# Kernel tuning notes

Hardware: AMD Instinct MI355X
Metric: run time of the kernel (lower is better)

The kernel has to match this reference:

```python
import jax, jax.numpy as jnp
import numpy as np

E = 8        # num experts
K = 2        # top-k
B, L, D = 2, 2048, 2048
I = 768      # moe expert intermediate size
IS = 4096    # shared expert intermediate size


def setup_inputs() -> dict:
    key = jax.random.key(0)
    ks = jax.random.split(key, 8)
    s = 0.02
    return {
        "hidden_states": jax.random.normal(ks[0], (B, L, D), jnp.float32),
        "gate_w": jax.random.normal(ks[1], (E, D), jnp.float32) * s,
        "gate_up_proj": jax.random.normal(ks[2], (E, 2 * I, D), jnp.float32) * s,
        "down_proj": jax.random.normal(ks[3], (E, D, I), jnp.float32) * s,
        "shared_gate_w": jax.random.normal(ks[4], (IS, D), jnp.float32) * s,
        "shared_up_w": jax.random.normal(ks[5], (IS, D), jnp.float32) * s,
        "shared_down_w": jax.random.normal(ks[6], (D, IS), jnp.float32) * s,
        "shared_expert_gate_w": jax.random.normal(ks[7], (1, D), jnp.float32) * s,
    }


def reference(hidden_states, gate_w, gate_up_proj, down_proj,
              shared_gate_w, shared_up_w, shared_down_w, shared_expert_gate_w):
    Bb, Ll, Dd = hidden_states.shape
    h = hidden_states.reshape(-1, Dd)                         # [T, D]
    silu = jax.nn.silu

    # shared expert: SiLU-gated MLP, scaled by sigmoid scalar gate
    shared = (silu(h @ shared_gate_w.T) * (h @ shared_up_w.T)) @ shared_down_w.T
    shared_out = jax.nn.sigmoid(h @ shared_expert_gate_w.T) * shared   # [T, D]

    # router: softmax over all experts, top-k, renormalize
    logits = h @ gate_w.T                                     # [T, E]
    probs = jax.nn.softmax(logits, axis=-1)
    topk_w, topk_idx = jax.lax.top_k(probs, K)                # [T, K]
    topk_w = topk_w / jnp.sum(topk_w, axis=-1, keepdims=True)

    # combine weights per (token, expert); zero for unselected experts,
    # so the dense per-expert compute below matches the gather/scatter loop.
    cw = jnp.sum(jax.nn.one_hot(topk_idx, E, dtype=h.dtype) * topk_w[..., None], axis=1)  # [T, E]

    # grouped gated MLP over all experts (dense dispatch)
    gu = jnp.einsum('td,efd->tef', h, gate_up_proj)           # [T, E, 2I]
    g, u = jnp.split(gu, 2, axis=-1)
    act = silu(g) * u                                         # [T, E, I]
    out = jnp.einsum('tei,edi->ted', act, down_proj)          # [T, E, D]
    partial = jnp.einsum('ted,te->td', out, cw)               # [T, D]

    return (partial + shared_out).reshape(Bb, Ll, Dd)
```

## Files before the change

### kernel.cpp

```cpp
#include <hip/hip_runtime.h>


#define T_TOK 4096
#define DIM   2048
#define NEXP  8
#define IEXP  768
#define ISHR  4096

typedef __attribute__((ext_vector_type(8))) short bf16x8_t;
typedef __attribute__((ext_vector_type(4))) float f32x4_t;

__device__ __forceinline__ unsigned short f2bf(float f) {
    unsigned int u = __float_as_uint(f);
    u += 0x7fffu + ((u >> 16) & 1u);
    return (unsigned short)(u >> 16);
}

__device__ __forceinline__ void gl2lds16(const unsigned short* g, unsigned short* l) {
    __builtin_amdgcn_global_load_lds(
        (const __attribute__((address_space(1))) unsigned int*)g,
        (__attribute__((address_space(3))) unsigned int*)l, 16, 0, 0);
}

#define C0 6291456
#define C1 9437184
#define C2 11534336
#define C3 13631488
#define C4 15728640
__global__ __launch_bounds__(256) void fused_cast_kernel(
    const float* __restrict__ s0, const float* __restrict__ s1,
    const float* __restrict__ s2, const float* __restrict__ s3,
    const float* __restrict__ s4,
    unsigned short* __restrict__ d0, unsigned short* __restrict__ d1,
    unsigned short* __restrict__ d2, unsigned short* __restrict__ d3,
    unsigned short* __restrict__ d4, int* __restrict__ cnt) {
    if (blockIdx.x == 0 && threadIdx.x < NEXP) cnt[threadIdx.x] = 0;
    int i = blockIdx.x * 256 + threadIdx.x;
    const float* src; unsigned short* dst; int base;
    if      (i < C0) { src = s0; dst = d0; base = 0;  }
    else if (i < C1) { src = s1; dst = d1; base = C0; }
    else if (i < C2) { src = s2; dst = d2; base = C1; }
    else if (i < C3) { src = s3; dst = d3; base = C2; }
    else             { src = s4; dst = d4; base = C3; }
    int j = i - base;
    float4 v = ((const float4*)src)[j];
    short4 r;
    r.x = (short)f2bf(v.x); r.y = (short)f2bf(v.y);
    r.z = (short)f2bf(v.z); r.w = (short)f2bf(v.w);
    ((short4*)dst)[j] = r;
}

__global__ __launch_bounds__(256) void router_kernel(
    const float* __restrict__ h, const float* __restrict__ gw,
    const float* __restrict__ segw,
    unsigned short* __restrict__ h_bf,
    float* __restrict__ sig, int* __restrict__ cnt,
    int* __restrict__ enc, float* __restrict__ wl) {
    int w = threadIdx.x >> 6, l = threadIdx.x & 63;
    int t = blockIdx.x * 4 + w;
    float p[9];
#pragma unroll
    for (int e = 0; e < 9; ++e) p[e] = 0.f;
    const float* hr = h + (size_t)t * DIM;
    unsigned short* hb = h_bf + (size_t)t * DIM;
    for (int i = 0; i < DIM; i += 64) {
        float x = hr[i + l];
        hb[i + l] = f2bf(x);
#pragma unroll
        for (int e = 0; e < NEXP; ++e) p[e] += x * gw[e * DIM + i + l];
        p[8] += x * segw[i + l];
    }
#pragma unroll
    for (int off = 32; off > 0; off >>= 1) {
#pragma unroll
        for (int e = 0; e < 9; ++e) p[e] += __shfl_xor(p[e], off, 64);
    }
    if (l == 0) {
        int b1 = 0; float v1 = p[0];
        for (int e = 1; e < NEXP; ++e) if (p[e] > v1) { v1 = p[e]; b1 = e; }
        int b2 = -1; float v2 = -1e30f;
        for (int e = 0; e < NEXP; ++e)
            if (e != b1 && p[e] > v2) { v2 = p[e]; b2 = e; }
        float w1 = 1.f / (1.f + __expf(v2 - v1));
        int pos = atomicAdd(&cnt[b1], 1);
        enc[b1 * T_TOK + pos] = 2 * t;     wl[b1 * T_TOK + pos] = w1;
        pos = atomicAdd(&cnt[b2], 1);
        enc[b2 * T_TOK + pos] = 2 * t + 1; wl[b2 * T_TOK + pos] = 1.f - w1;
        sig[t] = 1.f / (1.f + __expf(-p[8]));
    }
}


__global__ __launch_bounds__(64, 2) void gemm_gateup_all(
    const unsigned short* __restrict__ hA,
    const unsigned short* __restrict__ wsg, const unsigned short* __restrict__ wsu,
    const unsigned short* __restrict__ wgu,
    const int* __restrict__ enc, const int* __restrict__ cnt_arr,
    unsigned short* __restrict__ act_s, unsigned short* __restrict__ act_e) {
    int z = blockIdx.z;
    const unsigned short *Wg, *Wu;
    const int* lst; int cnt, gc0, ldo;
    unsigned short* outp;
    if (z < 128) {
        gc0 = z * 32; Wg = wsg; Wu = wsu;
        lst = nullptr; cnt = T_TOK; outp = act_s; ldo = ISHR;
    } else {
        int zz = z - 128;
        int e = zz / 24, ny = zz % 24;
        gc0 = ny * 32;
        Wg = wgu + (size_t)e * 2 * IEXP * DIM;
        Wu = Wg + (size_t)IEXP * DIM;
        lst = enc + e * T_TOK; cnt = cnt_arr[e];
        outp = act_e + (size_t)e * T_TOK * IEXP; ldo = IEXP;
    }
    int m0 = blockIdx.x * 64;
    if (m0 >= cnt) return;

    __shared__ __align__(16) unsigned short As[64 * 64];
    __shared__ __align__(16) unsigned short Bs[64 * 64];

    int l = threadIdx.x;
    int subrow = l >> 3;
    int chunk8 = ((l & 7) ^ subrow) << 3;

    unsigned aoff[8];
    unsigned boff[8];
#pragma unroll
    for (int c = 0; c < 8; ++c) {
        int row = 8 * c + subrow;
        int pp = m0 + row; if (pp >= cnt) pp = cnt - 1;
        int tk = lst ? (lst[pp] >> 1) : pp;
        aoff[c] = (unsigned)(tk * DIM + chunk8);
        int rg = row >> 4;
        int wrow = gc0 + ((rg >> 1) << 4) + (row & 15);
        boff[c] = (unsigned)(wrow * DIM + chunk8);
    }

    f32x4_t zero4 = {0.f, 0.f, 0.f, 0.f};
    f32x4_t acc[4][4];
#pragma unroll
    for (int i = 0; i < 4; ++i)
#pragma unroll
        for (int j = 0; j < 4; ++j) acc[i][j] = zero4;

    int lane15 = l & 15, q = l >> 4;

#pragma unroll
    for (int c = 0; c < 8; ++c) {
        gl2lds16(hA + aoff[c], &As[c * 512]);
        gl2lds16((((c >> 1) & 1) ? Wu : Wg) + boff[c], &Bs[c * 512]);
    }

    const int NK = DIM / 64;
    for (int t = 0; t < NK; ++t) {
        asm volatile("s_waitcnt vmcnt(0)" ::: "memory");
        __builtin_amdgcn_sched_barrier(0);
        bf16x8_t a[4][2], b[4][2];
#pragma unroll
        for (int i = 0; i < 4; ++i) {
            int R = 16 * i + lane15;
            int base = R * 64;
            int sx = (R & 7) << 3;
#pragma unroll
            for (int kk = 0; kk < 2; ++kk) {
                int cx = (((kk * 4 + q) << 3) ^ sx);
                a[i][kk] = *(const bf16x8_t*)&As[base + cx];
                b[i][kk] = *(const bf16x8_t*)&Bs[base + cx];
            }
        }
        asm volatile("s_waitcnt lgkmcnt(0)" ::: "memory");
        __builtin_amdgcn_sched_barrier(0);
        if (t + 1 < NK) {
            int k1 = (t + 1) * 64;
#pragma unroll
            for (int c = 0; c < 8; ++c) {
                gl2lds16(hA + aoff[c] + k1, &As[c * 512]);
                gl2lds16((((c >> 1) & 1) ? Wu : Wg) + boff[c] + k1, &Bs[c * 512]);
            }
        }
        __builtin_amdgcn_sched_barrier(0);
#pragma unroll
        for (int kk = 0; kk < 2; ++kk)
#pragma unroll
            for (int i = 0; i < 4; ++i)
#pragma unroll
                for (int j = 0; j < 4; ++j)
                    acc[i][j] = __builtin_amdgcn_mfma_f32_16x16x32_bf16(
                        a[i][kk], b[j][kk], acc[i][j], 0, 0, 0);
    }

#pragma unroll
    for (int i = 0; i < 4; ++i) {
#pragma unroll
        for (int r = 0; r < 4; ++r) {
            int p = m0 + 16 * i + 4 * q + r;
            unsigned short* orow = outp + (size_t)p * ldo + gc0 + lane15;
            float g0 = acc[i][0][r], u0 = acc[i][1][r];
            float g1 = acc[i][2][r], u1 = acc[i][3][r];
            orow[0]  = f2bf((g0 / (1.f + __expf(-g0))) * u0);
            orow[16] = f2bf((g1 / (1.f + __expf(-g1))) * u1);
        }
    }
}

__global__ __launch_bounds__(64, 2) void gemm_down_shared(
    const unsigned short* __restrict__ act_s,
    const unsigned short* __restrict__ wsd,
    const float* __restrict__ sig,
    float* __restrict__ out) {
    int m0 = blockIdx.x * 64;
    int n0 = blockIdx.y * 64;

    __shared__ __align__(16) unsigned short As[64 * 64];
    __shared__ __align__(16) unsigned short Bs[64 * 64];

    int l = threadIdx.x;
    int subrow = l >> 3;
    int chunk8 = ((l & 7) ^ subrow) << 3;

    unsigned aoff[8], boff[8];
#pragma unroll
    for (int c = 0; c < 8; ++c) {
        int row = 8 * c + subrow;
        aoff[c] = (unsigned)((m0 + row) * ISHR + chunk8);
        boff[c] = (unsigned)((n0 + row) * ISHR + chunk8);
    }

    f32x4_t zero4 = {0.f, 0.f, 0.f, 0.f};
    f32x4_t acc[4][4];
#pragma unroll
    for (int i = 0; i < 4; ++i)
#pragma unroll
        for (int j = 0; j < 4; ++j) acc[i][j] = zero4;

    int lane15 = l & 15, q = l >> 4;

#pragma unroll
    for (int c = 0; c < 8; ++c) {
        gl2lds16(act_s + aoff[c], &As[c * 512]);
        gl2lds16(wsd + boff[c], &Bs[c * 512]);
    }

    const int NK = ISHR / 64;
    for (int t = 0; t < NK; ++t) {
        asm volatile("s_waitcnt vmcnt(0)" ::: "memory");
        __builtin_amdgcn_sched_barrier(0);
        bf16x8_t a[4][2], b[4][2];
#pragma unroll
        for (int i = 0; i < 4; ++i) {
            int R = 16 * i + lane15;
            int base = R * 64;
            int sx = (R & 7) << 3;
#pragma unroll
            for (int kk = 0; kk < 2; ++kk) {
                int cx = (((kk * 4 + q) << 3) ^ sx);
                a[i][kk] = *(const bf16x8_t*)&As[base + cx];
                b[i][kk] = *(const bf16x8_t*)&Bs[base + cx];
            }
        }
        asm volatile("s_waitcnt lgkmcnt(0)" ::: "memory");
        __builtin_amdgcn_sched_barrier(0);
        if (t + 1 < NK) {
            int k1 = (t + 1) * 64;
#pragma unroll
            for (int c = 0; c < 8; ++c) {
                gl2lds16(act_s + aoff[c] + k1, &As[c * 512]);
                gl2lds16(wsd + boff[c] + k1, &Bs[c * 512]);
            }
        }
        __builtin_amdgcn_sched_barrier(0);
#pragma unroll
        for (int kk = 0; kk < 2; ++kk)
#pragma unroll
            for (int i = 0; i < 4; ++i)
#pragma unroll
                for (int j = 0; j < 4; ++j)
                    acc[i][j] = __builtin_amdgcn_mfma_f32_16x16x32_bf16(
                        a[i][kk], b[j][kk], acc[i][j], 0, 0, 0);
    }

#pragma unroll
    for (int i = 0; i < 4; ++i) {
#pragma unroll
        for (int r = 0; r < 4; ++r) {
            int p = m0 + 16 * i + 4 * q + r;
            float sc = sig[p];
            float* orow = out + (size_t)p * DIM + n0 + lane15;
#pragma unroll
            for (int j = 0; j < 4; ++j)
                orow[16 * j] = sc * acc[i][j][r];
        }
    }
}

__global__ __launch_bounds__(64, 2) void gemm_down_expert(
    const unsigned short* __restrict__ act_e,
    const unsigned short* __restrict__ wdn,
    const int* __restrict__ enc, const int* __restrict__ cnt_arr,
    const float* __restrict__ wlst,
    float* __restrict__ out) {
    int e = blockIdx.z;
    const unsigned short* A = act_e + (size_t)e * T_TOK * IEXP;
    const unsigned short* W = wdn + (size_t)e * DIM * IEXP;
    const int* lst = enc + e * T_TOK;
    const float* scl = wlst + (size_t)e * T_TOK;
    int cnt = cnt_arr[e];
    int m0 = blockIdx.x * 64;
    if (m0 >= cnt) return;
    int n0 = blockIdx.y * 64;

    __shared__ __align__(16) unsigned short As[64 * 64];
    __shared__ __align__(16) unsigned short Bs[64 * 64];

    int l = threadIdx.x;
    int subrow = l >> 3;
    int chunk8 = ((l & 7) ^ subrow) << 3;

    unsigned aoff[8], boff[8];
#pragma unroll
    for (int c = 0; c < 8; ++c) {
        int row = 8 * c + subrow;
        int pp = m0 + row; if (pp >= cnt) pp = cnt - 1;
        aoff[c] = (unsigned)(pp * IEXP + chunk8);
        boff[c] = (unsigned)((n0 + row) * IEXP + chunk8);
    }

    f32x4_t zero4 = {0.f, 0.f, 0.f, 0.f};
    f32x4_t acc[4][4];
#pragma unroll
    for (int i = 0; i < 4; ++i)
#pragma unroll
        for (int j = 0; j < 4; ++j) acc[i][j] = zero4;

    int lane15 = l & 15, q = l >> 4;

#pragma unroll
    for (int c = 0; c < 8; ++c) {
        gl2lds16(A + aoff[c], &As[c * 512]);
        gl2lds16(W + boff[c], &Bs[c * 512]);
    }

    const int NK = IEXP / 64;
    for (int t = 0; t < NK; ++t) {
        asm volatile("s_waitcnt vmcnt(0)" ::: "memory");
        __builtin_amdgcn_sched_barrier(0);
        bf16x8_t a[4][2], b[4][2];
#pragma unroll
        for (int i = 0; i < 4; ++i) {
            int R = 16 * i + lane15;
            int base = R * 64;
            int sx = (R & 7) << 3;
#pragma unroll
            for (int kk = 0; kk < 2; ++kk) {
                int cx = (((kk * 4 + q) << 3) ^ sx);
                a[i][kk] = *(const bf16x8_t*)&As[base + cx];
                b[i][kk] = *(const bf16x8_t*)&Bs[base + cx];
            }
        }
        asm volatile("s_waitcnt lgkmcnt(0)" ::: "memory");
        __builtin_amdgcn_sched_barrier(0);
        if (t + 1 < NK) {
            int k1 = (t + 1) * 64;
#pragma unroll
            for (int c = 0; c < 8; ++c) {
                gl2lds16(A + aoff[c] + k1, &As[c * 512]);
                gl2lds16(W + boff[c] + k1, &Bs[c * 512]);
            }
        }
        __builtin_amdgcn_sched_barrier(0);
#pragma unroll
        for (int kk = 0; kk < 2; ++kk)
#pragma unroll
            for (int i = 0; i < 4; ++i)
#pragma unroll
                for (int j = 0; j < 4; ++j)
                    acc[i][j] = __builtin_amdgcn_mfma_f32_16x16x32_bf16(
                        a[i][kk], b[j][kk], acc[i][j], 0, 0, 0);
    }

#pragma unroll
    for (int i = 0; i < 4; ++i) {
#pragma unroll
        for (int r = 0; r < 4; ++r) {
            int p = m0 + 16 * i + 4 * q + r;
            if (p < cnt) {
                int dest = lst[p] >> 1;
                float sc = scl[p];
                float* orow = out + (size_t)dest * DIM + n0 + lane15;
#pragma unroll
                for (int j = 0; j < 4; ++j)
                    atomicAdd(&orow[16 * j], sc * acc[i][j][r]);
            }
        }
    }
}

extern "C" void kernel_launch(void* const* d_in, const int* in_sizes, int n_in,
                              void* d_out, int out_size, void* d_ws, size_t ws_size,
                              hipStream_t stream) {
    (void)in_sizes; (void)n_in; (void)out_size; (void)ws_size;
    const float* h    = (const float*)d_in[0];
    const float* gw   = (const float*)d_in[1];
    const float* gup  = (const float*)d_in[2];
    const float* dnp  = (const float*)d_in[3];
    const float* sgw  = (const float*)d_in[4];
    const float* suw  = (const float*)d_in[5];
    const float* sdw  = (const float*)d_in[6];
    const float* segw = (const float*)d_in[7];
    float* out = (float*)d_out;

    char* ws = (char*)d_ws;
    size_t off = 0;
    auto alloc = [&](size_t bytes) {
        void* p = ws + off;
        off += (bytes + 255) & ~(size_t)255;
        return p;
    };
    unsigned short* h_bf   = (unsigned short*)alloc((size_t)T_TOK * DIM * 2);
    unsigned short* wgu_bf = (unsigned short*)alloc((size_t)NEXP * 2 * IEXP * DIM * 2);
    unsigned short* wdn_bf = (unsigned short*)alloc((size_t)NEXP * DIM * IEXP * 2);
    unsigned short* wsg_bf = (unsigned short*)alloc((size_t)ISHR * DIM * 2);
    unsigned short* wsu_bf = (unsigned short*)alloc((size_t)ISHR * DIM * 2);
    unsigned short* wsd_bf = (unsigned short*)alloc((size_t)DIM * ISHR * 2);
    unsigned short* act_s  = (unsigned short*)alloc((size_t)T_TOK * ISHR * 2);
    unsigned short* act_e  = (unsigned short*)alloc((size_t)NEXP * T_TOK * IEXP * 2);
    float* sig     = (float*)alloc((size_t)T_TOK * 4);
    int*   cnt     = (int*)alloc(NEXP * 4);
    int*   enc     = (int*)alloc((size_t)NEXP * T_TOK * 4);
    float* wl      = (float*)alloc((size_t)NEXP * T_TOK * 4);

    fused_cast_kernel<<<C4 / 256, 256, 0, stream>>>(
        gup, dnp, sgw, suw, sdw,
        wgu_bf, wdn_bf, wsg_bf, wsu_bf, wsd_bf, cnt);

    router_kernel<<<T_TOK / 4, 256, 0, stream>>>(
        h, gw, segw, h_bf, sig, cnt, enc, wl);

    gemm_gateup_all<<<dim3(T_TOK / 64, 1, 128 + 24 * NEXP), 64, 0, stream>>>(
        h_bf, wsg_bf, wsu_bf, wgu_bf, enc, cnt, act_s, act_e);

    gemm_down_shared<<<dim3(T_TOK / 64, DIM / 64, 1), 64, 0, stream>>>(
        act_s, wsd_bf, sig, out);

    gemm_down_expert<<<dim3(T_TOK / 64, DIM / 64, NEXP), 64, 0, stream>>>(
        act_e, wdn_bf, enc, cnt, wl, out);
}
```

Before: 900.3 us.

## Widen GEMM tiles to 64x128 with XCD-aware block remap and MFMA priority

New measurement: 754.9 us. 1.19x faster.

```diff
diff --git a/kernel.cpp b/kernel.cpp
--- a/kernel.cpp
+++ b/kernel.cpp
@@ -97,96 +97,107 @@
     const unsigned short* __restrict__ wgu,
     const int* __restrict__ enc, const int* __restrict__ cnt_arr,
     unsigned short* __restrict__ act_s, unsigned short* __restrict__ act_e) {
-    int z = blockIdx.z;
+    unsigned g = blockIdx.x;
+    unsigned xcd = g & 7, slot = g >> 3;
+    unsigned z = (slot >> 6) * 8 + xcd;
+    unsigned x = slot & 63;
+
     const unsigned short *Wg, *Wu;
     const int* lst; int cnt, gc0, ldo;
     unsigned short* outp;
-    if (z < 128) {
-        gc0 = z * 32; Wg = wsg; Wu = wsu;
+    if (z < 64) {
+        gc0 = z * 64; Wg = wsg; Wu = wsu;
         lst = nullptr; cnt = T_TOK; outp = act_s; ldo = ISHR;
     } else {
-        int zz = z - 128;
-        int e = zz / 24, ny = zz % 24;
-        gc0 = ny * 32;
+        int zz = z - 64;
+        int e = zz / 12, ny = zz % 12;
+        gc0 = ny * 64;
         Wg = wgu + (size_t)e * 2 * IEXP * DIM;
         Wu = Wg + (size_t)IEXP * DIM;
         lst = enc + e * T_TOK; cnt = cnt_arr[e];
         outp = act_e + (size_t)e * T_TOK * IEXP; ldo = IEXP;
     }
-    int m0 = blockIdx.x * 64;
+    int m0 = x * 64;
     if (m0 >= cnt) return;
 
     __shared__ __align__(16) unsigned short As[64 * 64];
-    __shared__ __align__(16) unsigned short Bs[64 * 64];
+    __shared__ __align__(16) unsigned short Bs[128 * 64];
 
     int l = threadIdx.x;
     int subrow = l >> 3;
     int chunk8 = ((l & 7) ^ subrow) << 3;
 
     unsigned aoff[8];
-    unsigned boff[8];
 #pragma unroll
     for (int c = 0; c < 8; ++c) {
         int row = 8 * c + subrow;
         int pp = m0 + row; if (pp >= cnt) pp = cnt - 1;
         int tk = lst ? (lst[pp] >> 1) : pp;
         aoff[c] = (unsigned)(tk * DIM + chunk8);
-        int rg = row >> 4;
-        int wrow = gc0 + ((rg >> 1) << 4) + (row & 15);
+    }
+    unsigned boff[16];
+#pragma unroll
+    for (int c = 0; c < 16; ++c) {
+        int wrow = gc0 + 16 * (c >> 2) + 8 * (c & 1) + subrow;
         boff[c] = (unsigned)(wrow * DIM + chunk8);
     }
 
     f32x4_t zero4 = {0.f, 0.f, 0.f, 0.f};
-    f32x4_t acc[4][4];
+    f32x4_t acc[4][8];
 #pragma unroll
     for (int i = 0; i < 4; ++i)
 #pragma unroll
-        for (int j = 0; j < 4; ++j) acc[i][j] = zero4;
+        for (int j = 0; j < 8; ++j) acc[i][j] = zero4;
 
     int lane15 = l & 15, q = l >> 4;
-
-#pragma unroll
-    for (int c = 0; c < 8; ++c) {
-        gl2lds16(hA + aoff[c], &As[c * 512]);
+    int sx = (lane15 & 7) << 3;
+    int cxk0 = (q << 3) ^ sx;
+    int cxk1 = ((4 + q) << 3) ^ sx;
+
+#pragma unroll
+    for (int c = 0; c < 8; ++c) gl2lds16(hA + aoff[c], &As[c * 512]);
+#pragma unroll
+    for (int c = 0; c < 16; ++c)
         gl2lds16((((c >> 1) & 1) ? Wu : Wg) + boff[c], &Bs[c * 512]);
-    }
 
     const int NK = DIM / 64;
     for (int t = 0; t < NK; ++t) {
         asm volatile("s_waitcnt vmcnt(0)" ::: "memory");
         __builtin_amdgcn_sched_barrier(0);
-        bf16x8_t a[4][2], b[4][2];
-#pragma unroll
-        for (int i = 0; i < 4; ++i) {
-            int R = 16 * i + lane15;
-            int base = R * 64;
-            int sx = (R & 7) << 3;
-#pragma unroll
-            for (int kk = 0; kk < 2; ++kk) {
-                int cx = (((kk * 4 + q) << 3) ^ sx);
-                a[i][kk] = *(const bf16x8_t*)&As[base + cx];
-                b[i][kk] = *(const bf16x8_t*)&Bs[base + cx];
+#pragma unroll
+        for (int kk = 0; kk < 2; ++kk) {
+            int cx = kk ? cxk1 : cxk0;
+            bf16x8_t a[4], b[8];
+#pragma unroll
+            for (int i = 0; i < 4; ++i)
+                a[i] = *(const bf16x8_t*)&As[1024 * i + lane15 * 64 + cx];
+#pragma unroll
+            for (int j = 0; j < 8; ++j)
+                b[j] = *(const bf16x8_t*)&Bs[1024 * j + lane15 * 64 + cx];
+            if (kk == 1) {
+                asm volatile("s_waitcnt lgkmcnt(0)" ::: "memory");
+                __builtin_amdgcn_sched_barrier(0);
+                if (t + 1 < NK) {
+                    int k1 = (t + 1) * 64;
+#pragma unroll
+                    for (int c = 0; c < 8; ++c)
+                        gl2lds16(hA + aoff[c] + k1, &As[c * 512]);
+#pragma unroll
+                    for (int c = 0; c < 16; ++c)
+                        gl2lds16((((c >> 1) & 1) ? Wu : Wg) + boff[c] + k1,
+                                 &Bs[c * 512]);
+                }
+                __builtin_amdgcn_sched_barrier(0);
             }
-        }
-        asm volatile("s_waitcnt lgkmcnt(0)" ::: "memory");
-        __builtin_amdgcn_sched_barrier(0);
-        if (t + 1 < NK) {
-            int k1 = (t + 1) * 64;
-#pragma unroll
-            for (int c = 0; c < 8; ++c) {
-                gl2lds16(hA + aoff[c] + k1, &As[c * 512]);
-                gl2lds16((((c >> 1) & 1) ? Wu : Wg) + boff[c] + k1, &Bs[c * 512]);
-            }
-        }
-        __builtin_amdgcn_sched_barrier(0);
-#pragma unroll
-        for (int kk = 0; kk < 2; ++kk)
-#pragma unroll
-            for (int i = 0; i < 4; ++i)
-#pragma unroll
-                for (int j = 0; j < 4; ++j)
+            __builtin_amdgcn_s_setprio(1);
+#pragma unroll
+            for (int i = 0; i < 4; ++i)
+#pragma unroll
+                for (int j = 0; j < 8; ++j)
                     acc[i][j] = __builtin_amdgcn_mfma_f32_16x16x32_bf16(
-                        a[i][kk], b[j][kk], acc[i][j], 0, 0, 0);
+                        a[i], b[j], acc[i][j], 0, 0, 0);
+            __builtin_amdgcn_s_setprio(0);
+        }
     }
 
 #pragma unroll
@@ -195,10 +206,12 @@
         for (int r = 0; r < 4; ++r) {
             int p = m0 + 16 * i + 4 * q + r;
             unsigned short* orow = outp + (size_t)p * ldo + gc0 + lane15;
-            float g0 = acc[i][0][r], u0 = acc[i][1][r];
-            float g1 = acc[i][2][r], u1 = acc[i][3][r];
-            orow[0]  = f2bf((g0 / (1.f + __expf(-g0))) * u0);
-            orow[16] = f2bf((g1 / (1.f + __expf(-g1))) * u1);
+#pragma unroll
+            for (int m = 0; m < 4; ++m) {
+                float gg = acc[i][2 * m][r];
+                float uu = acc[i][2 * m + 1][r];
+                orow[16 * m] = f2bf((gg / (1.f + __expf(-gg))) * uu);
+            }
         }
     }
 }
@@ -208,75 +221,83 @@
     const unsigned short* __restrict__ wsd,
     const float* __restrict__ sig,
     float* __restrict__ out) {
-    int m0 = blockIdx.x * 64;
-    int n0 = blockIdx.y * 64;
+    unsigned g = blockIdx.x;
+    unsigned xcd = g & 7, slot = g >> 3;
+    unsigned y = (slot >> 6) * 8 + xcd;
+    unsigned x = slot & 63;
+    int m0 = x * 64;
+    int n0 = y * 128;
 
     __shared__ __align__(16) unsigned short As[64 * 64];
-    __shared__ __align__(16) unsigned short Bs[64 * 64];
+    __shared__ __align__(16) unsigned short Bs[128 * 64];
 
     int l = threadIdx.x;
     int subrow = l >> 3;
     int chunk8 = ((l & 7) ^ subrow) << 3;
 
-    unsigned aoff[8], boff[8];
-#pragma unroll
-    for (int c = 0; c < 8; ++c) {
-        int row = 8 * c + subrow;
-        aoff[c] = (unsigned)((m0 + row) * ISHR + chunk8);
-        boff[c] = (unsigned)((n0 + row) * ISHR + chunk8);
-    }
+    unsigned aoff[8];
+#pragma unroll
+    for (int c = 0; c < 8; ++c)
+        aoff[c] = (unsigned)((m0 + 8 * c + subrow) * ISHR + chunk8);
+    unsigned boff[16];
+#pragma unroll
+    for (int c = 0; c < 16; ++c)
+        boff[c] = (unsigned)((n0 + 8 * c + subrow) * ISHR + chunk8);
 
     f32x4_t zero4 = {0.f, 0.f, 0.f, 0.f};
-    f32x4_t acc[4][4];
+    f32x4_t acc[4][8];
 #pragma unroll
     for (int i = 0; i < 4; ++i)
 #pragma unroll
-        for (int j = 0; j < 4; ++j) acc[i][j] = zero4;
+        for (int j = 0; j < 8; ++j) acc[i][j] = zero4;
 
     int lane15 = l & 15, q = l >> 4;
-
-#pragma unroll
-    for (int c = 0; c < 8; ++c) {
-        gl2lds16(act_s + aoff[c], &As[c * 512]);
-        gl2lds16(wsd + boff[c], &Bs[c * 512]);
-    }
+    int sx = (lane15 & 7) << 3;
+    int cxk0 = (q << 3) ^ sx;
+    int cxk1 = ((4 + q) << 3) ^ sx;
+
+#pragma unroll
+    for (int c = 0; c < 8; ++c) gl2lds16(act_s + aoff[c], &As[c * 512]);
+#pragma unroll
+    for (int c = 0; c < 16; ++c) gl2lds16(wsd + boff[c], &Bs[c * 512]);
 
     const int NK = ISHR / 64;
     for (int t = 0; t < NK; ++t) {
         asm volatile("s_waitcnt vmcnt(0)" ::: "memory");
         __builtin_amdgcn_sched_barrier(0);
-        bf16x8_t a[4][2], b[4][2];
-#pragma unroll
-        for (int i = 0; i < 4; ++i) {
-            int R = 16 * i + lane15;
-            int base = R * 64;
-            int sx = (R & 7) << 3;
-#pragma unroll
-            for (int kk = 0; kk < 2; ++kk) {
-                int cx = (((kk * 4 + q) << 3) ^ sx);
-                a[i][kk] = *(const bf16x8_t*)&As[base + cx];
-                b[i][kk] = *(const bf16x8_t*)&Bs[base + cx];
+#pragma unroll
+        for (int kk = 0; kk < 2; ++kk) {
+            int cx = kk ? cxk1 : cxk0;
+            bf16x8_t a[4], b[8];
+#pragma unroll
+            for (int i = 0; i < 4; ++i)
+                a[i] = *(const bf16x8_t*)&As[1024 * i + lane15 * 64 + cx];
+#pragma unroll
+            for (int j = 0; j < 8; ++j)
+                b[j] = *(const bf16x8_t*)&Bs[1024 * j + lane15 * 64 + cx];
+            if (kk == 1) {
+                asm volatile("s_waitcnt lgkmcnt(0)" ::: "memory");
+                __builtin_amdgcn_sched_barrier(0);
+                if (t + 1 < NK) {
+                    int k1 = (t + 1) * 64;
+#pragma unroll
+                    for (int c = 0; c < 8; ++c)
+                        gl2lds16(act_s + aoff[c] + k1, &As[c * 512]);
+#pragma unroll
+                    for (int c = 0; c < 16; ++c)
+                        gl2lds16(wsd + boff[c] + k1, &Bs[c * 512]);
+                }
+                __builtin_amdgcn_sched_barrier(0);
             }
-        }
-        asm volatile("s_waitcnt lgkmcnt(0)" ::: "memory");
-        __builtin_amdgcn_sched_barrier(0);
-        if (t + 1 < NK) {
-            int k1 = (t + 1) * 64;
-#pragma unroll
-            for (int c = 0; c < 8; ++c) {
-                gl2lds16(act_s + aoff[c] + k1, &As[c * 512]);
-                gl2lds16(wsd + boff[c] + k1, &Bs[c * 512]);
-            }
-        }
-        __builtin_amdgcn_sched_barrier(0);
-#pragma unroll
-        for (int kk = 0; kk < 2; ++kk)
-#pragma unroll
-            for (int i = 0; i < 4; ++i)
-#pragma unroll
-                for (int j = 0; j < 4; ++j)
+            __builtin_amdgcn_s_setprio(1);
+#pragma unroll
+            for (int i = 0; i < 4; ++i)
+#pragma unroll
+                for (int j = 0; j < 8; ++j)
                     acc[i][j] = __builtin_amdgcn_mfma_f32_16x16x32_bf16(
-                        a[i][kk], b[j][kk], acc[i][j], 0, 0, 0);
+                        a[i], b[j], acc[i][j], 0, 0, 0);
+            __builtin_amdgcn_s_setprio(0);
+        }
     }
 
 #pragma unroll
@@ -287,7 +308,7 @@
             float sc = sig[p];
             float* orow = out + (size_t)p * DIM + n0 + lane15;
 #pragma unroll
-            for (int j = 0; j < 4; ++j)
+            for (int j = 0; j < 8; ++j)
                 orow[16 * j] = sc * acc[i][j][r];
         }
     }
@@ -299,83 +320,93 @@
     const int* __restrict__ enc, const int* __restrict__ cnt_arr,
     const float* __restrict__ wlst,
     float* __restrict__ out) {
-    int e = blockIdx.z;
+    unsigned g = blockIdx.x;
+    unsigned xcd = g & 7, slot = g >> 3;
+    unsigned panel = (slot >> 6) * 8 + xcd;
+    unsigned x = slot & 63;
+    int e = panel >> 4, y = panel & 15;
+
     const unsigned short* A = act_e + (size_t)e * T_TOK * IEXP;
     const unsigned short* W = wdn + (size_t)e * DIM * IEXP;
     const int* lst = enc + e * T_TOK;
     const float* scl = wlst + (size_t)e * T_TOK;
     int cnt = cnt_arr[e];
-    int m0 = blockIdx.x * 64;
+    int m0 = x * 64;
     if (m0 >= cnt) return;
-    int n0 = blockIdx.y * 64;
+    int n0 = y * 128;
 
     __shared__ __align__(16) unsigned short As[64 * 64];
-    __shared__ __align__(16) unsigned short Bs[64 * 64];
+    __shared__ __align__(16) unsigned short Bs[128 * 64];
 
     int l = threadIdx.x;
     int subrow = l >> 3;
     int chunk8 = ((l & 7) ^ subrow) << 3;
 
-    unsigned aoff[8], boff[8];
+    unsigned aoff[8];
 #pragma unroll
     for (int c = 0; c < 8; ++c) {
-        int row = 8 * c + subrow;
-        int pp = m0 + row; if (pp >= cnt) pp = cnt - 1;
+        int pp = m0 + 8 * c + subrow; if (pp >= cnt) pp = cnt - 1;
         aoff[c] = (unsigned)(pp * IEXP + chunk8);
-        boff[c] = (unsigned)((n0 + row) * IEXP + chunk8);
-    }
+    }
+    unsigned boff[16];
+#pragma unroll
+    for (int c = 0; c < 16; ++c)
+        boff[c] = (unsigned)((n0 + 8 * c + subrow) * IEXP + chunk8);
 
     f32x4_t zero4 = {0.f, 0.f, 0.f, 0.f};
-    f32x4_t acc[4][4];
+    f32x4_t acc[4][8];
 #pragma unroll
     for (int i = 0; i < 4; ++i)
 #pragma unroll
-        for (int j = 0; j < 4; ++j) acc[i][j] = zero4;
+        for (int j = 0; j < 8; ++j) acc[i][j] = zero4;
 
     int lane15 = l & 15, q = l >> 4;
-
-#pragma unroll
-    for (int c = 0; c < 8; ++c) {
-        gl2lds16(A + aoff[c], &As[c * 512]);
-        gl2lds16(W + boff[c], &Bs[c * 512]);
-    }
+    int sx = (lane15 & 7) << 3;
+    int cxk0 = (q << 3) ^ sx;
+    int cxk1 = ((4 + q) << 3) ^ sx;
+
+#pragma unroll
+    for (int c = 0; c < 8; ++c) gl2lds16(A + aoff[c], &As[c * 512]);
+#pragma unroll
+    for (int c = 0; c < 16; ++c) gl2lds16(W + boff[c], &Bs[c * 512]);
 
     const int NK = IEXP / 64;
     for (int t = 0; t < NK; ++t) {
         asm volatile("s_waitcnt vmcnt(0)" ::: "memory");
         __builtin_amdgcn_sched_barrier(0);
-        bf16x8_t a[4][2], b[4][2];
-#pragma unroll
-        for (int i = 0; i < 4; ++i) {
-            int R = 16 * i + lane15;
-            int base = R * 64;
-            int sx = (R & 7) << 3;
-#pragma unroll
-            for (int kk = 0; kk < 2; ++kk) {
-                int cx = (((kk * 4 + q) << 3) ^ sx);
-                a[i][kk] = *(const bf16x8_t*)&As[base + cx];
-                b[i][kk] = *(const bf16x8_t*)&Bs[base + cx];
+#pragma unroll
+        for (int kk = 0; kk < 2; ++kk) {
+            int cx = kk ? cxk1 : cxk0;
+            bf16x8_t a[4], b[8];
+#pragma unroll
+            for (int i = 0; i < 4; ++i)
+                a[i] = *(const bf16x8_t*)&As[1024 * i + lane15 * 64 + cx];
+#pragma unroll
+            for (int j = 0; j < 8; ++j)
+                b[j] = *(const bf16x8_t*)&Bs[1024 * j + lane15 * 64 + cx];
+            if (kk == 1) {
+                asm volatile("s_waitcnt lgkmcnt(0)" ::: "memory");
+                __builtin_amdgcn_sched_barrier(0);
+                if (t + 1 < NK) {
+                    int k1 = (t + 1) * 64;
+#pragma unroll
+                    for (int c = 0; c < 8; ++c)
+                        gl2lds16(A + aoff[c] + k1, &As[c * 512]);
+#pragma unroll
+                    for (int c = 0; c < 16; ++c)
+                        gl2lds16(W + boff[c] + k1, &Bs[c * 512]);
+                }
+                __builtin_amdgcn_sched_barrier(0);
             }
-        }
-        asm volatile("s_waitcnt lgkmcnt(0)" ::: "memory");
-        __builtin_amdgcn_sched_barrier(0);
-        if (t + 1 < NK) {
-            int k1 = (t + 1) * 64;
-#pragma unroll
-            for (int c = 0; c < 8; ++c) {
-                gl2lds16(A + aoff[c] + k1, &As[c * 512]);
-                gl2lds16(W + boff[c] + k1, &Bs[c * 512]);
-            }
-        }
-        __builtin_amdgcn_sched_barrier(0);
-#pragma unroll
-        for (int kk = 0; kk < 2; ++kk)
-#pragma unroll
-            for (int i = 0; i < 4; ++i)
-#pragma unroll
-                for (int j = 0; j < 4; ++j)
+            __builtin_amdgcn_s_setprio(1);
+#pragma unroll
+            for (int i = 0; i < 4; ++i)
+#pragma unroll
+                for (int j = 0; j < 8; ++j)
                     acc[i][j] = __builtin_amdgcn_mfma_f32_16x16x32_bf16(
-                        a[i][kk], b[j][kk], acc[i][j], 0, 0, 0);
+                        a[i], b[j], acc[i][j], 0, 0, 0);
+            __builtin_amdgcn_s_setprio(0);
+        }
     }
 
 #pragma unroll
@@ -388,7 +419,7 @@
                 float sc = scl[p];
                 float* orow = out + (size_t)dest * DIM + n0 + lane15;
 #pragma unroll
-                for (int j = 0; j < 4; ++j)
+                for (int j = 0; j < 8; ++j)
                     atomicAdd(&orow[16 * j], sc * acc[i][j][r]);
             }
         }
@@ -436,12 +467,12 @@
     router_kernel<<<T_TOK / 4, 256, 0, stream>>>(
         h, gw, segw, h_bf, sig, cnt, enc, wl);
 
-    gemm_gateup_all<<<dim3(T_TOK / 64, 1, 128 + 24 * NEXP), 64, 0, stream>>>(
+    gemm_gateup_all<<<160 * 64, 64, 0, stream>>>(
         h_bf, wsg_bf, wsu_bf, wgu_bf, enc, cnt, act_s, act_e);
 
-    gemm_down_shared<<<dim3(T_TOK / 64, DIM / 64, 1), 64, 0, stream>>>(
+    gemm_down_shared<<<16 * 64, 64, 0, stream>>>(
         act_s, wsd_bf, sig, out);
 
-    gemm_down_expert<<<dim3(T_TOK / 64, DIM / 64, NEXP), 64, 0, stream>>>(
+    gemm_down_expert<<<128 * 64, 64, 0, stream>>>(
         act_e, wdn_bf, enc, cnt, wl, out);
 }
```
